# Kernel optimization log

Hardware: AMD Instinct MI355X
Metric: run time of the kernel (lower is better)

Reference implementation:

```python
import jax, jax.numpy as jnp
import numpy as np

MEMORY_SIZE = 512
PATTERN_DIM = 256
NUM_WAVELENGTHS = 3
ATTENTION_FOCUS = 1.0
CORRELATION_THRESHOLD = 0.3
H_NOISE = 0.03  # noise scale for the holographic medium buffer


def setup_inputs() -> dict:
    key = jax.random.key(0)
    k1, k2, k3 = jax.random.split(key, 3)
    B, R = 32, 128  # batch, rows per stimulus (R * PATTERN_DIM flat features)
    stimulus = jax.random.normal(k1, (B, R * PATTERN_DIM), dtype=jnp.float32)
    H_real = jax.random.normal(k2, (MEMORY_SIZE, PATTERN_DIM, NUM_WAVELENGTHS), dtype=jnp.float32) * H_NOISE
    H_imag = jax.random.normal(k3, (MEMORY_SIZE, PATTERN_DIM, NUM_WAVELENGTHS), dtype=jnp.float32) * H_NOISE
    return {"stimulus": stimulus, "H_real": H_real, "H_imag": H_imag}


def reference(stimulus, H_real, H_imag):
    # Faithful 'retrieve' mode of HolographicAssociativeMemory, fully vectorized.
    B = stimulus.shape[0]
    q = stimulus.reshape(B, -1, PATTERN_DIM).astype(jnp.complex64)  # [B, R, P]
    qf = jnp.fft.fft2(q, axes=(-2, -1))                             # [B, R, P]
    R = qf.shape[1]

    # query_fft[b, mem_idx % R] for every memory slot -> gather rows
    rows = jnp.arange(MEMORY_SIZE) % R
    q_rows = qf[:, rows, :]                                         # [B, M, P]

    H = (H_real + 1j * H_imag).astype(jnp.complex64)                # [M, P, W]
    phases = jnp.linspace(0.0, 2.0 * np.pi, NUM_WAVELENGTHS).astype(jnp.float32)
    ref_beams = jnp.exp(1j * phases).astype(jnp.complex64)          # [W]

    # reconstruction = query_fft_row * stored_hologram * reference_beam
    recon = q_rows[:, :, :, None] * H[None, :, :, :] * ref_beams    # [B, M, P, W]
    # torch.fft.ifft2 on a (1, P) tensor == ifft along P (size-1 axis is identity)
    rec = jnp.fft.ifft(recon, axis=2)                               # [B, M, P, W]
    corr = jnp.abs(rec).mean(axis=2)                                # [B, M, W]
    avg_corr = corr.mean(axis=-1)                                   # [B, M]

    focused = avg_corr * jnp.float32(ATTENTION_FOCUS)
    retrieved = jnp.where(focused > jnp.float32(CORRELATION_THRESHOLD), focused, jnp.float32(0.0))
    return retrieved
```

## Files before the change

### kernel.cpp

```cpp
#include <hip/hip_runtime.h>
#include <math.h>


#define TWO_PI 6.28318530717958647692f
#define PI_F   3.14159265358979323846f

#if __has_builtin(__builtin_amdgcn_permlane16_swap)
#define USE_PL16 1
#else
#define USE_PL16 0
#endif
#if __has_builtin(__builtin_amdgcn_permlane32_swap)
#define USE_PL32 1
#else
#define USE_PL32 0
#endif

typedef float f2 __attribute__((ext_vector_type(2)));
typedef unsigned int uint2v __attribute__((ext_vector_type(2)));

__device__ inline f2 mkf2(float x, float y) { f2 r; r[0] = x; r[1] = y; return r; }

__device__ inline f2 cmul(f2 a, f2 b) {
    const f2 axx = __builtin_shufflevector(a, a, 0, 0);
    const f2 ayn = mkf2(-a[1], a[1]);
    const f2 byx = __builtin_shufflevector(b, b, 1, 0);
    return axx * b + ayn * byx;
}
__device__ inline f2 csq(f2 a) { return cmul(a, a); }
__device__ inline f2 ab2(f2 A, f2 v, f2 B, f2 o) {
    const f2 Axx = __builtin_shufflevector(A, A, 0, 0);
    const f2 Ayn = mkf2(-A[1], A[1]);
    const f2 Bxx = __builtin_shufflevector(B, B, 0, 0);
    const f2 Byn = mkf2(-B[1], B[1]);
    const f2 vyx = __builtin_shufflevector(v, v, 1, 0);
    const f2 oyx = __builtin_shufflevector(o, o, 1, 0);
    return Axx * v + Ayn * vyx + Bxx * o + Byn * oyx;
}
__device__ inline f2 cfma2(f2 S, f2 b, f2 a) {
    const f2 Sxx = __builtin_shufflevector(S, S, 0, 0);
    const f2 Syn = mkf2(-S[1], S[1]);
    const f2 byx = __builtin_shufflevector(b, b, 1, 0);
    return Sxx * b + (Syn * byx + a);
}
__device__ inline f2 shfl_xor_c(f2 v, int mask) {
    return mkf2(__shfl_xor(v[0], mask, 64), __shfl_xor(v[1], mask, 64));
}

#define DPP_XOR1 0xB1
#define DPP_XOR2 0x4E
template <int CTRL>
__device__ inline f2 dpp_quad(f2 v) {
    return mkf2(
        __int_as_float(__builtin_amdgcn_update_dpp(__float_as_int(v[0]), __float_as_int(v[0]),
                                                   CTRL, 0xF, 0xF, false)),
        __int_as_float(__builtin_amdgcn_update_dpp(__float_as_int(v[1]), __float_as_int(v[1]),
                                                   CTRL, 0xF, 0xF, false)));
}

#if USE_PL16
__device__ inline void swap16c(f2 v, f2& a, f2& b) {
    uint2v rx = __builtin_amdgcn_permlane16_swap(__float_as_uint(v[0]), __float_as_uint(v[0]), false, false);
    uint2v ry = __builtin_amdgcn_permlane16_swap(__float_as_uint(v[1]), __float_as_uint(v[1]), false, false);
    a = mkf2(__uint_as_float(rx[0]), __uint_as_float(ry[0]));
    b = mkf2(__uint_as_float(rx[1]), __uint_as_float(ry[1]));
}
#endif
#if USE_PL32
__device__ inline void swap32c(f2 v, f2& a, f2& b) {
    uint2v rx = __builtin_amdgcn_permlane32_swap(__float_as_uint(v[0]), __float_as_uint(v[0]), false, false);
    uint2v ry = __builtin_amdgcn_permlane32_swap(__float_as_uint(v[1]), __float_as_uint(v[1]), false, false);
    a = mkf2(__uint_as_float(rx[0]), __uint_as_float(ry[0]));
    b = mkf2(__uint_as_float(rx[1]), __uint_as_float(ry[1]));
}
#endif

__global__ __launch_bounds__(256) void k_prep(const float* __restrict__ x,
                                              f2* __restrict__ y,
                                              const float* __restrict__ Hr,
                                              const float* __restrict__ Hi,
                                              f2* __restrict__ Ht) {
    if (blockIdx.x >= 1024) {
        const int idx = (blockIdx.x - 1024) * 256 + threadIdx.x;
        const int m = idx / 768;
        const int rem = idx - m * 768;
        const int w = rem >> 8;
        const int p = rem & 255;
        const int k = __brev((unsigned)p) >> 24;
        const int src = (m * 256 + k) * 3 + w;
        Ht[idx] = mkf2(Hr[src], Hi[src]);
        return;
    }

    const int lane = threadIdx.x & 63;
    const int wid  = blockIdx.x * 4 + (threadIdx.x >> 6);
    float sn, cs;

    __sincosf(-PI_F * (float)lane * (1.0f / 128.0f), &sn, &cs);
    const f2 gam    = mkf2(cs, sn);
    const f2 w128_0 = gam;
    const f2 w128_1 = mkf2(gam[1], -gam[0]);
    const f2 w64f = csq(gam);
    const f2 g4   = csq(w64f);
    const f2 g8   = csq(g4);
    const f2 g16  = csq(g8);
    const f2 g32  = csq(g16);
    const f2 g64  = csq(g32);
    const f2 one  = mkf2(1.0f, 0.0f);
#if USE_PL32
    const f2 P32 = (lane & 32) ? mkf2(-g4[0], -g4[1]) : one;
    const f2 Q32 = (lane & 32) ? g4 : one;
#else
    const f2 A32f = (lane & 32) ? g4 : one;
    const f2 B32f = (lane & 32) ? mkf2(-g4[0], -g4[1]) : one;
#endif
#if USE_PL16
    const f2 P16 = (lane & 16) ? mkf2(-g8[0], -g8[1]) : one;
    const f2 Q16 = (lane & 16) ? g8 : one;
#else
    const f2 A16f = (lane & 16) ? g8 : one;
    const f2 B16f = (lane & 16) ? mkf2(-g8[0], -g8[1]) : one;
#endif
    const f2 A8f = (lane & 8) ? g16 : one;
    const f2 B8f = (lane & 8) ? mkf2(-g16[0], -g16[1]) : one;
    const f2 A4f = (lane & 4) ? g32 : one;
    const f2 B4f = (lane & 4) ? mkf2(-g32[0], -g32[1]) : one;
    const f2 A2f = (lane & 2) ? g64 : one;
    const f2 B2f = (lane & 2) ? mkf2(-g64[0], -g64[1]) : one;
    const f2 sg1 = (lane & 1) ? mkf2(-1.0f, -1.0f) : mkf2(1.0f, 1.0f);

    const float* xr = x + (size_t)wid * 256;
    f2 v[4];
    v[0] = mkf2(xr[lane],       0.0f);
    v[1] = mkf2(xr[64 + lane],  0.0f);
    v[2] = mkf2(xr[128 + lane], 0.0f);
    v[3] = mkf2(xr[192 + lane], 0.0f);

    { f2 a = v[0], bq = v[2]; v[0] = a + bq; v[2] = cmul(a - bq, w128_0); }
    { f2 a = v[1], bq = v[3]; v[1] = a + bq; v[3] = cmul(a - bq, w128_1); }
    { f2 a = v[0], bq = v[1]; v[0] = a + bq; v[1] = cmul(a - bq, w64f); }
    { f2 a = v[2], bq = v[3]; v[2] = a + bq; v[3] = cmul(a - bq, w64f); }

#pragma unroll
    for (int j = 0; j < 4; ++j) {
#if USE_PL32
        f2 a, bb; swap32c(v[j], a, bb);
        v[j] = ab2(P32, a, Q32, bb);
#else
        const f2 o = shfl_xor_c(v[j], 32);
        v[j] = ab2(A32f, v[j], B32f, o);
#endif
    }
#pragma unroll
    for (int j = 0; j < 4; ++j) {
#if USE_PL16
        f2 a, bb; swap16c(v[j], a, bb);
        v[j] = ab2(P16, a, Q16, bb);
#else
        const f2 o = shfl_xor_c(v[j], 16);
        v[j] = ab2(A16f, v[j], B16f, o);
#endif
    }
#pragma unroll
    for (int j = 0; j < 4; ++j) {
        const f2 o = shfl_xor_c(v[j], 8);
        v[j] = ab2(A8f, v[j], B8f, o);
    }
#pragma unroll
    for (int j = 0; j < 4; ++j) {
        const f2 o = shfl_xor_c(v[j], 4);
        v[j] = ab2(A4f, v[j], B4f, o);
    }
#pragma unroll
    for (int j = 0; j < 4; ++j) {
        const f2 o = dpp_quad<DPP_XOR2>(v[j]);
        v[j] = ab2(A2f, v[j], B2f, o);
    }
#pragma unroll
    for (int j = 0; j < 4; ++j) {
        const f2 o = dpp_quad<DPP_XOR1>(v[j]);
        v[j] = sg1 * v[j] + o;
    }

    f2* yr = y + (size_t)wid * 256;
#pragma unroll
    for (int j = 0; j < 4; ++j) yr[j * 64 + lane] = v[j];
}

__global__ __launch_bounds__(256) void k_fft_cols(f2* __restrict__ y) {
    __shared__ f2 sm[128][17];
    __shared__ f2 tw[64];
    const int tid = threadIdx.x;

    if (tid < 64) {
        float sn, cs;
        __sincosf(-TWO_PI * (float)tid * (1.0f / 128.0f), &sn, &cs);
        tw[tid] = mkf2(cs, sn);
    }

    const int b  = blockIdx.x >> 4;
    const int d0 = (blockIdx.x & 15) << 4;
    const int c  = tid & 15;
    const int r0 = tid >> 4;
    const size_t base = ((size_t)b * 128) * 256 + (size_t)d0 + (size_t)c;

#pragma unroll
    for (int r = r0; r < 128; r += 16) {
        sm[__brev((unsigned)r) >> 25][c] = y[base + (size_t)r * 256];
    }
    __syncthreads();

#pragma unroll
    for (int st = 0; st < 7; ++st) {
        const int half = 1 << st;
#pragma unroll
        for (int k = 0; k < 4; ++k) {
            const int idx = tid + (k << 8);
            const int cc  = idx & 15;
            const int j   = idx >> 4;
            const int pos = j & (half - 1);
            const int i0  = (j << 1) - pos;
            const int i1  = i0 + half;
            const f2 w  = tw[pos << (6 - st)];
            const f2 a  = sm[i0][cc];
            const f2 bv = cmul(sm[i1][cc], w);
            sm[i0][cc] = a + bv;
            sm[i1][cc] = a - bv;
        }
        __syncthreads();
    }

#pragma unroll
    for (int r = r0; r < 128; r += 16) {
        y[base + (size_t)r * 256] = sm[r][c];
    }
}

__global__ __launch_bounds__(256) void k_recon(const f2* __restrict__ qf,
                                               const f2* __restrict__ Ht,
                                               float* __restrict__ out) {
    const int lane = threadIdx.x & 63;
    const int task = blockIdx.x * 4 + (threadIdx.x >> 6);
    const int b = task >> 9;
    const int m = task & 511;
    const int r = m & 127;

    const f2* q = qf + ((size_t)(b * 128 + r)) * 256;
    f2 qv[4];
#pragma unroll
    for (int j = 0; j < 4; ++j) qv[j] = q[j * 64 + lane];

    float sn, cs;
    __sincosf(PI_F * (float)lane * (1.0f / 128.0f), &sn, &cs);
    const f2 wi0 = mkf2(cs, sn);
    const f2 w64 = csq(wi0);
    const f2 S32 = csq(w64);
    const f2 S16 = csq(S32);
    const f2 b16 = csq(S16);
    const f2 b32 = csq(b16);
    const f2 b64 = csq(b32);
    const f2 one = mkf2(1.0f, 0.0f);
    const f2 A8 = (lane & 8) ? b16 : one, B8 = (lane & 8) ? one : b16;
    const f2 A4 = (lane & 4) ? b32 : one, B4 = (lane & 4) ? one : b32;
    const f2 A2 = (lane & 2) ? b64 : one, B2 = (lane & 2) ? one : b64;
    const f2 sg1 = (lane & 1) ? mkf2(-1.0f, -1.0f) : mkf2(1.0f, 1.0f);
    const f2 wi1 = mkf2(-wi0[1], wi0[0]);
#if !USE_PL16
    const f2 A16 = (lane & 16) ? S16 : one, B16 = (lane & 16) ? one : S16;
#endif
#if !USE_PL32
    const f2 A32 = (lane & 32) ? S32 : one, B32 = (lane & 32) ? one : S32;
#endif

    const f2* hp = Ht + (size_t)m * 768;
    f2 v[3][4];
#pragma unroll
    for (int w = 0; w < 3; ++w)
#pragma unroll
        for (int j = 0; j < 4; ++j)
            v[w][j] = cmul(qv[j], hp[w * 256 + j * 64 + lane]);

#pragma unroll
    for (int w = 0; w < 3; ++w)
#pragma unroll
        for (int j = 0; j < 4; ++j) {
            const f2 o = dpp_quad<DPP_XOR1>(v[w][j]);
            v[w][j] = sg1 * v[w][j] + o;
        }
#pragma unroll
    for (int w = 0; w < 3; ++w)
#pragma unroll
        for (int j = 0; j < 4; ++j) {
            const f2 o = dpp_quad<DPP_XOR2>(v[w][j]);
            v[w][j] = ab2(A2, v[w][j], B2, o);
        }
#pragma unroll
    for (int w = 0; w < 3; ++w)
#pragma unroll
        for (int j = 0; j < 4; ++j) {
            const f2 o = shfl_xor_c(v[w][j], 4);
            v[w][j] = ab2(A4, v[w][j], B4, o);
        }
#pragma unroll
    for (int w = 0; w < 3; ++w)
#pragma unroll
        for (int j = 0; j < 4; ++j) {
            const f2 o = shfl_xor_c(v[w][j], 8);
            v[w][j] = ab2(A8, v[w][j], B8, o);
        }
#pragma unroll
    for (int w = 0; w < 3; ++w)
#pragma unroll
        for (int j = 0; j < 4; ++j) {
#if USE_PL16
            f2 a, bb; swap16c(v[w][j], a, bb);
            v[w][j] = cfma2(S16, bb, a);
#else
            const f2 o = shfl_xor_c(v[w][j], 16);
            v[w][j] = ab2(A16, v[w][j], B16, o);
#endif
        }
#pragma unroll
    for (int w = 0; w < 3; ++w)
#pragma unroll
        for (int j = 0; j < 4; ++j) {
#if USE_PL32
            f2 a, bb; swap32c(v[w][j], a, bb);
            v[w][j] = cfma2(S32, bb, a);
#else
            const f2 o = shfl_xor_c(v[w][j], 32);
            v[w][j] = ab2(A32, v[w][j], B32, o);
#endif
        }
#pragma unroll
    for (int w = 0; w < 3; ++w) {
        f2 tv = cmul(w64, v[w][1]);
        f2 a = v[w][0];
        v[w][0] = a + tv; v[w][1] = a - tv;
        tv = cmul(w64, v[w][3]);
        a = v[w][2];
        v[w][2] = a + tv; v[w][3] = a - tv;
        tv = cmul(wi0, v[w][2]);
        a = v[w][0];
        v[w][0] = a + tv; v[w][2] = a - tv;
        tv = cmul(wi1, v[w][3]);
        a = v[w][1];
        v[w][1] = a + tv; v[w][3] = a - tv;
    }

    float acc = 0.0f;
#pragma unroll
    for (int w = 0; w < 3; ++w)
#pragma unroll
        for (int j = 0; j < 4; ++j) {
            const f2 sq = v[w][j] * v[w][j];
            acc += __builtin_amdgcn_sqrtf(sq[0] + sq[1]);
        }

#pragma unroll
    for (int off = 32; off > 0; off >>= 1) acc += __shfl_xor(acc, off, 64);

    if (lane == 0) {
        const float focused = acc * (1.0f / (256.0f * 256.0f * 3.0f));
        out[task] = (focused > 0.3f) ? focused : 0.0f;
    }
}

extern "C" void kernel_launch(void* const* d_in, const int* in_sizes, int n_in,
                              void* d_out, int out_size, void* d_ws, size_t ws_size,
                              hipStream_t stream) {
    (void)in_sizes; (void)n_in; (void)out_size; (void)ws_size;
    const float* stim = (const float*)d_in[0];
    const float* Hr   = (const float*)d_in[1];
    const float* Hi   = (const float*)d_in[2];
    float* out = (float*)d_out;

    f2* y  = (f2*)d_ws;
    f2* Ht = (f2*)((char*)d_ws + (size_t)32 * 128 * 256 * sizeof(f2));

    k_prep<<<1024 + 1536, 256, 0, stream>>>(stim, y, Hr, Hi, Ht);
    k_fft_cols<<<32 * 16, 256, 0, stream>>>(y);
    k_recon<<<16384 / 4, 256, 0, stream>>>(y, Ht, out);
}
```

Before: 44.15 us.

## Reorder 2D FFT to columns-first and fuse row FFT into recon kernel

The column FFT now reads the real stimulus directly and runs first, together with the hologram transpose, in one launch. The row FFT moves into the recon kernel: one wave per block computes it and shares the result through LDS with the other waves. Each block handles the four memory slots that map to the same query row. This removes one kernel launch and one full round trip of the intermediate complex buffer through global memory. In exchange, three of the four waves in each recon block sit idle at a barrier while the row FFT runs.

Measured after the change: 40.92 us. 1.08x faster.

```diff
diff --git a/kernel.cpp b/kernel.cpp
--- a/kernel.cpp
+++ b/kernel.cpp
@@ -20,6 +20,7 @@
 typedef unsigned int uint2v __attribute__((ext_vector_type(2)));
 
 __device__ inline f2 mkf2(float x, float y) { f2 r; r[0] = x; r[1] = y; return r; }
+__device__ inline f2 conjf2(f2 a) { return mkf2(a[0], -a[1]); }
 
 __device__ inline f2 cmul(f2 a, f2 b) {
     const f2 axx = __builtin_shufflevector(a, a, 0, 0);
@@ -75,13 +76,13 @@
 }
 #endif
 
-__global__ __launch_bounds__(256) void k_prep(const float* __restrict__ x,
-                                              f2* __restrict__ y,
+__global__ __launch_bounds__(256) void k_cols(const float* __restrict__ x,
+                                              f2* __restrict__ yc,
                                               const float* __restrict__ Hr,
                                               const float* __restrict__ Hi,
                                               f2* __restrict__ Ht) {
-    if (blockIdx.x >= 1024) {
-        const int idx = (blockIdx.x - 1024) * 256 + threadIdx.x;
+    if (blockIdx.x >= 512) {
+        const int idx = (blockIdx.x - 512) * 256 + threadIdx.x;
         const int m = idx / 768;
         const int rem = idx - m * 768;
         const int w = rem >> 8;
@@ -92,102 +93,6 @@
         return;
     }
 
-    const int lane = threadIdx.x & 63;
-    const int wid  = blockIdx.x * 4 + (threadIdx.x >> 6);
-    float sn, cs;
-
-    __sincosf(-PI_F * (float)lane * (1.0f / 128.0f), &sn, &cs);
-    const f2 gam    = mkf2(cs, sn);
-    const f2 w128_0 = gam;
-    const f2 w128_1 = mkf2(gam[1], -gam[0]);
-    const f2 w64f = csq(gam);
-    const f2 g4   = csq(w64f);
-    const f2 g8   = csq(g4);
-    const f2 g16  = csq(g8);
-    const f2 g32  = csq(g16);
-    const f2 g64  = csq(g32);
-    const f2 one  = mkf2(1.0f, 0.0f);
-#if USE_PL32
-    const f2 P32 = (lane & 32) ? mkf2(-g4[0], -g4[1]) : one;
-    const f2 Q32 = (lane & 32) ? g4 : one;
-#else
-    const f2 A32f = (lane & 32) ? g4 : one;
-    const f2 B32f = (lane & 32) ? mkf2(-g4[0], -g4[1]) : one;
-#endif
-#if USE_PL16
-    const f2 P16 = (lane & 16) ? mkf2(-g8[0], -g8[1]) : one;
-    const f2 Q16 = (lane & 16) ? g8 : one;
-#else
-    const f2 A16f = (lane & 16) ? g8 : one;
-    const f2 B16f = (lane & 16) ? mkf2(-g8[0], -g8[1]) : one;
-#endif
-    const f2 A8f = (lane & 8) ? g16 : one;
-    const f2 B8f = (lane & 8) ? mkf2(-g16[0], -g16[1]) : one;
-    const f2 A4f = (lane & 4) ? g32 : one;
-    const f2 B4f = (lane & 4) ? mkf2(-g32[0], -g32[1]) : one;
-    const f2 A2f = (lane & 2) ? g64 : one;
-    const f2 B2f = (lane & 2) ? mkf2(-g64[0], -g64[1]) : one;
-    const f2 sg1 = (lane & 1) ? mkf2(-1.0f, -1.0f) : mkf2(1.0f, 1.0f);
-
-    const float* xr = x + (size_t)wid * 256;
-    f2 v[4];
-    v[0] = mkf2(xr[lane],       0.0f);
-    v[1] = mkf2(xr[64 + lane],  0.0f);
-    v[2] = mkf2(xr[128 + lane], 0.0f);
-    v[3] = mkf2(xr[192 + lane], 0.0f);
-
-    { f2 a = v[0], bq = v[2]; v[0] = a + bq; v[2] = cmul(a - bq, w128_0); }
-    { f2 a = v[1], bq = v[3]; v[1] = a + bq; v[3] = cmul(a - bq, w128_1); }
-    { f2 a = v[0], bq = v[1]; v[0] = a + bq; v[1] = cmul(a - bq, w64f); }
-    { f2 a = v[2], bq = v[3]; v[2] = a + bq; v[3] = cmul(a - bq, w64f); }
-
-#pragma unroll
-    for (int j = 0; j < 4; ++j) {
-#if USE_PL32
-        f2 a, bb; swap32c(v[j], a, bb);
-        v[j] = ab2(P32, a, Q32, bb);
-#else
-        const f2 o = shfl_xor_c(v[j], 32);
-        v[j] = ab2(A32f, v[j], B32f, o);
-#endif
-    }
-#pragma unroll
-    for (int j = 0; j < 4; ++j) {
-#if USE_PL16
-        f2 a, bb; swap16c(v[j], a, bb);
-        v[j] = ab2(P16, a, Q16, bb);
-#else
-        const f2 o = shfl_xor_c(v[j], 16);
-        v[j] = ab2(A16f, v[j], B16f, o);
-#endif
-    }
-#pragma unroll
-    for (int j = 0; j < 4; ++j) {
-        const f2 o = shfl_xor_c(v[j], 8);
-        v[j] = ab2(A8f, v[j], B8f, o);
-    }
-#pragma unroll
-    for (int j = 0; j < 4; ++j) {
-        const f2 o = shfl_xor_c(v[j], 4);
-        v[j] = ab2(A4f, v[j], B4f, o);
-    }
-#pragma unroll
-    for (int j = 0; j < 4; ++j) {
-        const f2 o = dpp_quad<DPP_XOR2>(v[j]);
-        v[j] = ab2(A2f, v[j], B2f, o);
-    }
-#pragma unroll
-    for (int j = 0; j < 4; ++j) {
-        const f2 o = dpp_quad<DPP_XOR1>(v[j]);
-        v[j] = sg1 * v[j] + o;
-    }
-
-    f2* yr = y + (size_t)wid * 256;
-#pragma unroll
-    for (int j = 0; j < 4; ++j) yr[j * 64 + lane] = v[j];
-}
-
-__global__ __launch_bounds__(256) void k_fft_cols(f2* __restrict__ y) {
     __shared__ f2 sm[128][17];
     __shared__ f2 tw[64];
     const int tid = threadIdx.x;
@@ -202,11 +107,11 @@
     const int d0 = (blockIdx.x & 15) << 4;
     const int c  = tid & 15;
     const int r0 = tid >> 4;
-    const size_t base = ((size_t)b * 128) * 256 + (size_t)d0 + (size_t)c;
+    const size_t base = (size_t)b * 32768 + (size_t)d0 + (size_t)c;
 
 #pragma unroll
     for (int r = r0; r < 128; r += 16) {
-        sm[__brev((unsigned)r) >> 25][c] = y[base + (size_t)r * 256];
+        sm[__brev((unsigned)r) >> 25][c] = mkf2(x[base + (size_t)r * 256], 0.0f);
     }
     __syncthreads();
 
@@ -232,23 +137,19 @@
 
 #pragma unroll
     for (int r = r0; r < 128; r += 16) {
-        y[base + (size_t)r * 256] = sm[r][c];
-    }
-}
-
-__global__ __launch_bounds__(256) void k_recon(const f2* __restrict__ qf,
+        yc[base + (size_t)r * 256] = sm[r][c];
+    }
+}
+
+__global__ __launch_bounds__(256) void k_recon(const f2* __restrict__ yc,
                                                const f2* __restrict__ Ht,
                                                float* __restrict__ out) {
+    __shared__ f2 sh[256];
     const int lane = threadIdx.x & 63;
-    const int task = blockIdx.x * 4 + (threadIdx.x >> 6);
-    const int b = task >> 9;
-    const int m = task & 511;
-    const int r = m & 127;
-
-    const f2* q = qf + ((size_t)(b * 128 + r)) * 256;
-    f2 qv[4];
-#pragma unroll
-    for (int j = 0; j < 4; ++j) qv[j] = q[j * 64 + lane];
+    const int wid  = threadIdx.x >> 6;
+    const int b    = blockIdx.x >> 7;
+    const int r    = blockIdx.x & 127;
+    const int m    = r + (wid << 7);
 
     float sn, cs;
     __sincosf(PI_F * (float)lane * (1.0f / 128.0f), &sn, &cs);
@@ -272,6 +173,97 @@
     const f2 A32 = (lane & 32) ? S32 : one, B32 = (lane & 32) ? one : S32;
 #endif
 
+    if (wid == 0) {
+        const f2 gam    = conjf2(wi0);
+        const f2 w128_0 = gam;
+        const f2 w128_1 = mkf2(gam[1], -gam[0]);
+        const f2 w64f = conjf2(w64);
+        const f2 g4   = conjf2(S32);
+        const f2 g8   = conjf2(S16);
+        const f2 g16  = conjf2(b16);
+        const f2 g32  = conjf2(b32);
+        const f2 g64  = conjf2(b64);
+#if USE_PL32
+        const f2 P32 = (lane & 32) ? mkf2(-g4[0], -g4[1]) : one;
+        const f2 Q32 = (lane & 32) ? g4 : one;
+#else
+        const f2 A32f = (lane & 32) ? g4 : one;
+        const f2 B32f = (lane & 32) ? mkf2(-g4[0], -g4[1]) : one;
+#endif
+#if USE_PL16
+        const f2 P16 = (lane & 16) ? mkf2(-g8[0], -g8[1]) : one;
+        const f2 Q16 = (lane & 16) ? g8 : one;
+#else
+        const f2 A16f = (lane & 16) ? g8 : one;
+        const f2 B16f = (lane & 16) ? mkf2(-g8[0], -g8[1]) : one;
+#endif
+        const f2 A8f = (lane & 8) ? g16 : one;
+        const f2 B8f = (lane & 8) ? mkf2(-g16[0], -g16[1]) : one;
+        const f2 A4f = (lane & 4) ? g32 : one;
+        const f2 B4f = (lane & 4) ? mkf2(-g32[0], -g32[1]) : one;
+        const f2 A2f = (lane & 2) ? g64 : one;
+        const f2 B2f = (lane & 2) ? mkf2(-g64[0], -g64[1]) : one;
+
+        const f2* xr = yc + ((size_t)(b * 128 + r)) * 256;
+        f2 v[4];
+#pragma unroll
+        for (int j = 0; j < 4; ++j) v[j] = xr[j * 64 + lane];
+
+        { f2 a = v[0], bq = v[2]; v[0] = a + bq; v[2] = cmul(a - bq, w128_0); }
+        { f2 a = v[1], bq = v[3]; v[1] = a + bq; v[3] = cmul(a - bq, w128_1); }
+        { f2 a = v[0], bq = v[1]; v[0] = a + bq; v[1] = cmul(a - bq, w64f); }
+        { f2 a = v[2], bq = v[3]; v[2] = a + bq; v[3] = cmul(a - bq, w64f); }
+
+#pragma unroll
+        for (int j = 0; j < 4; ++j) {
+#if USE_PL32
+            f2 a, bb; swap32c(v[j], a, bb);
+            v[j] = ab2(P32, a, Q32, bb);
+#else
+            const f2 o = shfl_xor_c(v[j], 32);
+            v[j] = ab2(A32f, v[j], B32f, o);
+#endif
+        }
+#pragma unroll
+        for (int j = 0; j < 4; ++j) {
+#if USE_PL16
+            f2 a, bb; swap16c(v[j], a, bb);
+            v[j] = ab2(P16, a, Q16, bb);
+#else
+            const f2 o = shfl_xor_c(v[j], 16);
+            v[j] = ab2(A16f, v[j], B16f, o);
+#endif
+        }
+#pragma unroll
+        for (int j = 0; j < 4; ++j) {
+            const f2 o = shfl_xor_c(v[j], 8);
+            v[j] = ab2(A8f, v[j], B8f, o);
+        }
+#pragma unroll
+        for (int j = 0; j < 4; ++j) {
+            const f2 o = shfl_xor_c(v[j], 4);
+            v[j] = ab2(A4f, v[j], B4f, o);
+        }
+#pragma unroll
+        for (int j = 0; j < 4; ++j) {
+            const f2 o = dpp_quad<DPP_XOR2>(v[j]);
+            v[j] = ab2(A2f, v[j], B2f, o);
+        }
+#pragma unroll
+        for (int j = 0; j < 4; ++j) {
+            const f2 o = dpp_quad<DPP_XOR1>(v[j]);
+            v[j] = sg1 * v[j] + o;
+        }
+
+#pragma unroll
+        for (int j = 0; j < 4; ++j) sh[j * 64 + lane] = v[j];
+    }
+    __syncthreads();
+
+    f2 qv[4];
+#pragma unroll
+    for (int j = 0; j < 4; ++j) qv[j] = sh[j * 64 + lane];
+
     const f2* hp = Ht + (size_t)m * 768;
     f2 v[3][4];
 #pragma unroll
@@ -362,7 +354,7 @@
 
     if (lane == 0) {
         const float focused = acc * (1.0f / (256.0f * 256.0f * 3.0f));
-        out[task] = (focused > 0.3f) ? focused : 0.0f;
+        out[b * 512 + m] = (focused > 0.3f) ? focused : 0.0f;
     }
 }
 
@@ -375,10 +367,9 @@
     const float* Hi   = (const float*)d_in[2];
     float* out = (float*)d_out;
 
-    f2* y  = (f2*)d_ws;
+    f2* yc = (f2*)d_ws;
     f2* Ht = (f2*)((char*)d_ws + (size_t)32 * 128 * 256 * sizeof(f2));
 
-    k_prep<<<1024 + 1536, 256, 0, stream>>>(stim, y, Hr, Hi, Ht);
-    k_fft_cols<<<32 * 16, 256, 0, stream>>>(y);
-    k_recon<<<16384 / 4, 256, 0, stream>>>(y, Ht, out);
-}
+    k_cols<<<512 + 1536, 256, 0, stream>>>(stim, yc, Hr, Hi, Ht);
+    k_recon<<<4096, 256, 0, stream>>>(yc, Ht, out);
+}
```
